# Kernel tuning notes

Measured on AMD Instinct MI355X. Metric: run time of the kernel, lower is better.

Reference implementation:

```python
import jax, jax.numpy as jnp
import numpy as np

B, S, H, E = 32, 4096, 512, 512

def setup_inputs() -> dict:
    key = jax.random.key(0)
    ks = jax.random.split(key, 11)
    sc = 1.0 / np.sqrt(H)
    return {
        "context": jax.random.normal(ks[0], (B, S, H), jnp.float32),
        "h": jax.random.normal(ks[1], (B, H), jnp.float32),
        "x": jax.random.normal(ks[2], (B, E), jnp.float32),
        "We": jax.random.normal(ks[3], (H, H), jnp.float32) * sc,
        "be": jax.random.normal(ks[4], (H,), jnp.float32) * sc,
        "Wd": jax.random.normal(ks[5], (H, H), jnp.float32) * sc,
        "bd": jax.random.normal(ks[6], (H,), jnp.float32) * sc,
        "Wv": jax.random.normal(ks[7], (H,), jnp.float32) * sc,
        "bv": jax.random.normal(ks[8], (1,), jnp.float32) * sc,
        "Wr": jax.random.normal(ks[9], (2 * H, 2 * H + E), jnp.float32) * (1.0 / np.sqrt(2 * H + E)),
        "br": jax.random.normal(ks[10], (2 * H,), jnp.float32) * sc,
    }

def reference(context, h, x, We, be, Wd, bd, Wv, bv, Wr, br):
    # gamma_encoder: [B,S,H]; gamma_decoder: [B,1,H]
    ge = jnp.einsum('bsh,kh->bsk', context, We) + be
    gd = h @ Wd.T + bd
    # additive scores -> [B,S]
    scores = jnp.einsum('bsh,h->bs', jnp.tanh(ge + gd[:, None, :]), Wv) + bv[0]
    weights = jax.nn.softmax(scores, axis=1)
    # context vector c_t: [B,H]
    c_t = jnp.einsum('bs,bsh->bh', weights, context)
    # linear_r on [c_t, h, x] -> [B,2H]
    r_t = jnp.concatenate([c_t, h, x], axis=1) @ Wr.T + br
    # maxout over pairs: view [B,H,2].max(-1)
    output = jnp.max(r_t.reshape(-1, r_t.shape[1] // 2, 2), axis=2)
    return (output, weights)
```

## Files before the change

### kernel.cpp

```cpp
#include <hip/hip_runtime.h>

typedef __attribute__((ext_vector_type(8))) short bf16x8;
typedef __attribute__((ext_vector_type(16))) float f32x16;

typedef __attribute__((address_space(3))) unsigned int lds_u32;
typedef __attribute__((address_space(1))) unsigned int glb_u32;

__device__ inline unsigned int cvt_pk_bf16(float lo, float hi){
  unsigned int r;
  asm("v_cvt_pk_bf16_f32 %0, %1, %2" : "=v"(r) : "v"(lo), "v"(hi));
  return r;
}
__device__ inline bf16x8 pack8(float4 a, float4 b){
  union { unsigned int u[4]; bf16x8 v; } r;
  r.u[0]=cvt_pk_bf16(a.x,a.y); r.u[1]=cvt_pk_bf16(a.z,a.w);
  r.u[2]=cvt_pk_bf16(b.x,b.y); r.u[3]=cvt_pk_bf16(b.z,b.w);
  return r.v;
}
__device__ inline float fast_tanh(float x){
  float e = __builtin_amdgcn_exp2f(x * 2.8853900817779268f);
  return 1.0f - 2.0f * __builtin_amdgcn_rcpf(e + 1.0f);
}
#define LOG2E 1.4426950408889634f

__global__ __launch_bounds__(256) void we_conv(const float* __restrict__ We,
                                               uint4* __restrict__ weFrag){
  int gid = blockIdx.x * 256 + threadIdx.x;
  int l  = gid & 63;
  int hc = gid >> 10;
  int colv = (hc >> 1)*32 + (l & 31);
  int k = ((hc & 1) << 8) + ((gid >> 6) & 15)*16 + (l >> 5)*8;
  const float4* src = (const float4*)(We + colv*512 + k);
  float4 f0 = src[0], f1 = src[1];
  weFrag[gid] = make_uint4(cvt_pk_bf16(f0.x,f0.y), cvt_pk_bf16(f0.z,f0.w),
                           cvt_pk_bf16(f1.x,f1.y), cvt_pk_bf16(f1.z,f1.w));
}

__global__ __launch_bounds__(256) void gd_kernel(const float* __restrict__ hvec,
                                                 const float* __restrict__ Wd,
                                                 const float* __restrict__ bd,
                                                 const float* __restrict__ be,
                                                 float* __restrict__ gd){
  __shared__ float hs[512];
  int b = blockIdx.x >> 2, kc = blockIdx.x & 3;
  int tid = threadIdx.x;
  hs[tid]       = hvec[b*512 + tid];
  hs[tid + 256] = hvec[b*512 + 256 + tid];
  __syncthreads();
  int k  = kc*128 + (tid >> 1);
  int hh = (tid & 1) * 256;
  const float4* wrow = (const float4*)(Wd + (size_t)k*512 + hh);
  const float4* hv4  = (const float4*)(hs + hh);
  float acc = 0.f;
  #pragma unroll 8
  for (int i = 0; i < 64; ++i){
    float4 w = wrow[i]; float4 u = hv4[i];
    acc += w.x*u.x + w.y*u.y + w.z*u.z + w.w*u.w;
  }
  acc += __shfl_xor(acc, 1);
  if ((tid & 1) == 0) gd[b*512 + k] = acc + bd[k] + be[k];
}

__global__ __launch_bounds__(256, 2) void score_kernel(
    const float* __restrict__ ctx, const char* __restrict__ weFrag,
    const float* __restrict__ gd, const float* __restrict__ Wv,
    float* __restrict__ scores, unsigned int* __restrict__ ctp,
    float* __restrict__ MS){
  __shared__ char lds[40960];
  float* gdwv = (float*)(lds + 24576);
  float* scl  = (float*)(lds + 32768);
  float* wl   = (float*)(lds + 33280);
  float* redp = (float*)(lds + 33792);

  const int tid  = threadIdx.x;
  const int wid  = tid >> 6;
  const int lane = tid & 63;
  const int bid  = blockIdx.x;
  const int row0 = bid * 128;
  const int b    = bid >> 5;
  const int col  = lane & 31;
  const int hi   = lane >> 5;

  if (tid < 128) ((float4*)gdwv)[tid] = ((const float4*)(gd + b*512))[tid];
  else           ((float4*)gdwv)[tid] = ((const float4*)Wv)[tid - 128];

  bf16x8 afrag[32];
  {
    const float4* ap = (const float4*)(ctx + (size_t)(row0 + wid*32 + col)*512 + hi*8);
    #pragma unroll
    for (int t = 0; t < 32; ++t)
      afrag[t] = pack8(ap[t*4], ap[t*4 + 1]);
  }

  asm volatile("s_waitcnt lgkmcnt(0)" ::: "memory");

  #define ISSUE_Q(QC) do { \
    const char* _g = weFrag + ((size_t)((QC) >> 1))*16384 + ((QC) & 1)*8192 \
                     + wid*2048 + lane*16; \
    char* _l = lds + ((QC) % 3)*8192 + wid*2048; \
    __builtin_amdgcn_global_load_lds((const glb_u32*)_g, (lds_u32*)_l, 16, 0, 0); \
    __builtin_amdgcn_global_load_lds((const glb_u32*)(_g + 1024), \
                                     (lds_u32*)(_l + 1024), 16, 0, 0); \
  } while(0)

  ISSUE_Q(0);
  ISSUE_Q(1);

  f32x16 acc;
  float sc[16];
  #pragma unroll
  for (int r = 0; r < 16; ++r) sc[r] = 0.f;

  for (int nc = 0; nc < 16; ++nc){
    #pragma unroll
    for (int r = 0; r < 16; ++r) acc[r] = 0.f;

    #pragma unroll
    for (int j = 0; j < 4; ++j){
      const int qc = nc*4 + j;
      if (qc < 63) asm volatile("s_waitcnt vmcnt(2)" ::: "memory");
      else         asm volatile("s_waitcnt vmcnt(0)" ::: "memory");
      __builtin_amdgcn_s_barrier();
      if (qc < 62) ISSUE_Q(qc + 2);
      {
        const char* bb = lds + (qc % 3)*8192 + lane*16;
        __builtin_amdgcn_s_setprio(1);
        #pragma unroll
        for (int t = 0; t < 8; ++t){
          bf16x8 bf = *(const bf16x8*)(bb + t*1024);
          acc = __builtin_amdgcn_mfma_f32_32x32x16_bf16(afrag[j*8 + t], bf, acc, 0, 0, 0);
        }
        __builtin_amdgcn_s_setprio(0);
      }
    }

    float gdv = gdwv[nc*32 + col];
    float wvv = gdwv[512 + nc*32 + col];
    #pragma unroll
    for (int r = 0; r < 16; ++r)
      sc[r] += fast_tanh(acc[r] + gdv) * wvv;
  }
  #undef ISSUE_Q

  #pragma unroll
  for (int r = 0; r < 16; ++r){
    #pragma unroll
    for (int m = 1; m <= 16; m <<= 1) sc[r] += __shfl_xor(sc[r], m);
  }

  __syncthreads();
  if (col == 0){
    int rbase = wid*32 + 4*hi;
    float* so = scores + row0 + rbase;
    #pragma unroll
    for (int r = 0; r < 16; ++r){
      int rr = (r & 3) + 8*(r >> 2);
      so[rr] = sc[r];
      scl[rbase + rr] = sc[r];
    }
  }
  __syncthreads();

  float M = -1e30f;
  {
    const float4* s4 = (const float4*)scl;
    #pragma unroll
    for (int i = 0; i < 32; ++i){
      float4 v = s4[i];
      M = fmaxf(M, fmaxf(fmaxf(v.x, v.y), fmaxf(v.z, v.w)));
    }
  }
  if (tid < 128){
    float w = __builtin_amdgcn_exp2f((scl[tid] - M) * LOG2E);
    wl[tid] = w;
    #pragma unroll
    for (int o = 1; o < 64; o <<= 1) w += __shfl_xor(w, o);
    if ((tid & 63) == 0) redp[tid >> 6] = w;
  }
  __syncthreads();
  float S_blk = redp[0] + redp[1];

  float cA = 0.f, cB = 0.f;
  #pragma unroll
  for (int p = 0; p < 4; ++p){
    if (wid == p){
      int rl = col;
      char* dst = lds + rl*1024;
      int swz = (rl & 7) << 4;
      #pragma unroll
      for (int t = 0; t < 32; ++t){
        union { bf16x8 v; uint4 q; } u; u.v = afrag[t];
        *(uint4*)(dst + ((t*32 + hi*16) ^ swz)) = u.q;
      }
    }
    __syncthreads();
    const float* wp = wl + p*32;
    #pragma unroll 8
    for (int r = 0; r < 32; ++r){
      unsigned int u = *(const unsigned int*)(lds + r*1024 + ((tid*4) ^ ((r & 7) << 4)));
      float cw = wp[r];
      union { unsigned int q; float f; } flo, fhi;
      flo.q = u << 16;
      fhi.q = u & 0xffff0000u;
      cA += cw * flo.f;
      cB += cw * fhi.f;
    }
    __syncthreads();
  }
  ctp[(size_t)bid*256 + tid] = cvt_pk_bf16(cA, cB);
  if (tid == 0){ MS[2*bid] = M; MS[2*bid + 1] = S_blk; }
}

__global__ __launch_bounds__(256) void combine_kernel(const unsigned int* __restrict__ ctp,
                                                      const float* __restrict__ MS,
                                                      float* __restrict__ ct,
                                                      float* __restrict__ mbuf){
  __shared__ float wsh[32];
  __shared__ float msh[2];
  int b = blockIdx.x, tid = threadIdx.x;
  if (tid < 32){
    float Mi = MS[(b*32 + tid)*2];
    float Si = MS[(b*32 + tid)*2 + 1];
    float M = Mi;
    #pragma unroll
    for (int o = 1; o < 32; o <<= 1) M = fmaxf(M, __shfl_xor(M, o));
    float w = __builtin_amdgcn_exp2f((Mi - M) * LOG2E);
    float d = w * Si;
    #pragma unroll
    for (int o = 1; o < 32; o <<= 1) d += __shfl_xor(d, o);
    wsh[tid] = w;
    if (tid == 0){ msh[0] = M; msh[1] = 1.0f / d; }
  }
  __syncthreads();
  float invd = msh[1];
  float a0 = 0.f, a1 = 0.f;
  #pragma unroll 8
  for (int i = 0; i < 32; ++i){
    unsigned int u = ctp[(size_t)(b*32 + i)*256 + tid];
    float w = wsh[i];
    union { unsigned int q; float f; } flo, fhi;
    flo.q = u << 16;
    fhi.q = u & 0xffff0000u;
    a0 += w * flo.f;
    a1 += w * fhi.f;
  }
  ((float2*)(ct + b*512))[tid] = make_float2(a0 * invd, a1 * invd);
  if (tid == 0){ mbuf[2*b] = msh[0]; mbuf[2*b + 1] = invd; }
}

__global__ __launch_bounds__(256) void weights_kernel(const float* __restrict__ scores,
                                                      const float* __restrict__ mbuf,
                                                      float* __restrict__ weights){
  int b = blockIdx.x, tid = threadIdx.x;
  float M = mbuf[2*b], invd = mbuf[2*b + 1];
  const float4* src = (const float4*)(scores + b*4096);
  float4* dst = (float4*)(weights + b*4096);
  #pragma unroll
  for (int i = 0; i < 4; ++i){
    float4 v = src[tid + i*256];
    v.x = __builtin_amdgcn_exp2f((v.x - M) * LOG2E) * invd;
    v.y = __builtin_amdgcn_exp2f((v.y - M) * LOG2E) * invd;
    v.z = __builtin_amdgcn_exp2f((v.z - M) * LOG2E) * invd;
    v.w = __builtin_amdgcn_exp2f((v.w - M) * LOG2E) * invd;
    dst[tid + i*256] = v;
  }
}

__global__ __launch_bounds__(256) void final_kernel(
    const float* __restrict__ ct, const float* __restrict__ hvec,
    const float* __restrict__ x, const float* __restrict__ Wr,
    const float* __restrict__ br, float* __restrict__ out){
  __shared__ float xs[8][1536];
  int bt = blockIdx.x >> 4;
  int it = blockIdx.x & 15;
  int tid = threadIdx.x;
  int b0 = bt * 8;
  for (int idx = tid; idx < 8*1536; idx += 256){
    int bl = idx / 1536, j = idx % 1536;
    int b = b0 + bl;
    float v = (j < 512) ? ct[b*512 + j]
            : (j < 1024) ? hvec[b*512 + (j - 512)]
            : x[b*512 + (j - 1024)];
    xs[bl][j] = v;
  }
  __syncthreads();
  int i = it*64 + (tid & 63);
  int bl0 = (tid >> 6) * 2;
  const float4* wrow = (const float4*)(Wr + (size_t)i*1536);
  const float4* x0 = (const float4*)xs[bl0];
  const float4* x1 = (const float4*)xs[bl0 + 1];
  float a0 = 0.f, a1 = 0.f;
  #pragma unroll 4
  for (int k = 0; k < 384; ++k){
    float4 w = wrow[k];
    float4 u0 = x0[k], u1 = x1[k];
    a0 += w.x*u0.x + w.y*u0.y + w.z*u0.z + w.w*u0.w;
    a1 += w.x*u1.x + w.y*u1.y + w.z*u1.z + w.w*u1.w;
  }
  float bias = br[i];
  a0 += bias; a1 += bias;
  float n0 = __shfl_xor(a0, 1);
  float n1 = __shfl_xor(a1, 1);
  if ((tid & 1) == 0){
    out[(b0 + bl0    )*512 + (i >> 1)] = fmaxf(a0, n0);
    out[(b0 + bl0 + 1)*512 + (i >> 1)] = fmaxf(a1, n1);
  }
}

extern "C" void kernel_launch(void* const* d_in, const int* in_sizes, int n_in,
                              void* d_out, int out_size, void* d_ws, size_t ws_size,
                              hipStream_t stream){
  const float* ctx  = (const float*)d_in[0];
  const float* hvec = (const float*)d_in[1];
  const float* x    = (const float*)d_in[2];
  const float* We   = (const float*)d_in[3];
  const float* be   = (const float*)d_in[4];
  const float* Wd   = (const float*)d_in[5];
  const float* bd   = (const float*)d_in[6];
  const float* Wv   = (const float*)d_in[7];
  const float* Wr   = (const float*)d_in[9];
  const float* br   = (const float*)d_in[10];

  float* out     = (float*)d_out;
  float* weights = out + 32*512;

  char* ws = (char*)d_ws;
  char* weFrag   = ws;
  float* scores  = (float*)(ws + (512 << 10));
  unsigned int* ctp = (unsigned int*)(ws + (1024 << 10));
  float* MS      = (float*)(ws + (2 << 20));
  float* mbuf    = (float*)(ws + (2 << 20) + (16 << 10));
  float* ct      = (float*)(ws + (2 << 20) + (32 << 10));
  float* gd      = (float*)(ws + (2 << 20) + (96 << 10));

  we_conv<<<128, 256, 0, stream>>>(We, (uint4*)weFrag);
  gd_kernel<<<128, 256, 0, stream>>>(hvec, Wd, bd, be, gd);
  score_kernel<<<1024, 256, 0, stream>>>(ctx, weFrag, gd, Wv, scores, ctp, MS);
  combine_kernel<<<32, 256, 0, stream>>>(ctp, MS, ct, mbuf);
  weights_kernel<<<32, 256, 0, stream>>>(scores, mbuf, weights);
  final_kernel<<<64, 256, 0, stream>>>(ct, hvec, x, Wr, br, out);
}
```

Measured before the change: 194.1 us.

## Split score GEMM K dimension across two wave groups with 512-thread blocks

The score kernel now uses 512 threads per block. Each row group of 32 rows is handled by two waves that each cover half of the K dimension, so each wave holds 16 A fragments instead of 32, which cuts register pressure and allows more resident waves. Partial accumulators are combined through a new LDS exchange buffer before the tanh step, and the We fragment layout is reordered to match. The context partials are now stored as fp32 per column rather than packed bf16, which doubles that workspace and adds an extra barrier per N chunk.

```diff
diff --git a/kernel.cpp b/kernel.cpp
--- a/kernel.cpp
+++ b/kernel.cpp
@@ -26,10 +26,14 @@
 __global__ __launch_bounds__(256) void we_conv(const float* __restrict__ We,
                                                uint4* __restrict__ weFrag){
   int gid = blockIdx.x * 256 + threadIdx.x;
-  int l  = gid & 63;
-  int hc = gid >> 10;
-  int colv = (hc >> 1)*32 + (l & 31);
-  int k = ((hc & 1) << 8) + ((gid >> 6) & 15)*16 + (l >> 5)*8;
+  int l   = gid & 63;
+  int rec = gid >> 6;
+  int nc  = rec >> 5;
+  int q   = (rec >> 3) & 3;
+  int s   = rec & 7;
+  int t   = (s < 4) ? (q*4 + s) : (16 + q*4 + (s - 4));
+  int colv = nc*32 + (l & 31);
+  int k = t*16 + (l >> 5)*8;
   const float4* src = (const float4*)(We + colv*512 + k);
   float4 f0 = src[0], f1 = src[1];
   weFrag[gid] = make_uint4(cvt_pk_bf16(f0.x,f0.y), cvt_pk_bf16(f0.z,f0.w),
@@ -61,46 +65,47 @@
   if ((tid & 1) == 0) gd[b*512 + k] = acc + bd[k] + be[k];
 }
 
-__global__ __launch_bounds__(256, 2) void score_kernel(
+__global__ __launch_bounds__(512, 4) void score_kernel(
     const float* __restrict__ ctx, const char* __restrict__ weFrag,
     const float* __restrict__ gd, const float* __restrict__ Wv,
-    float* __restrict__ scores, unsigned int* __restrict__ ctp,
+    float* __restrict__ scores, float* __restrict__ ctp,
     float* __restrict__ MS){
-  __shared__ char lds[40960];
+  __shared__ char lds[46592];
   float* gdwv = (float*)(lds + 24576);
-  float* scl  = (float*)(lds + 32768);
-  float* wl   = (float*)(lds + 33280);
-  float* redp = (float*)(lds + 33792);
+  char*  xbuf = lds + 28672;
+  float* scl  = (float*)(lds + 45056);
+  float* wl   = (float*)(lds + 45568);
+  float* redp = (float*)(lds + 46080);
 
   const int tid  = threadIdx.x;
   const int wid  = tid >> 6;
   const int lane = tid & 63;
+  const int rg   = wid & 3;
+  const int kh   = wid >> 2;
   const int bid  = blockIdx.x;
   const int row0 = bid * 128;
   const int b    = bid >> 5;
   const int col  = lane & 31;
   const int hi   = lane >> 5;
 
-  if (tid < 128) ((float4*)gdwv)[tid] = ((const float4*)(gd + b*512))[tid];
-  else           ((float4*)gdwv)[tid] = ((const float4*)Wv)[tid - 128];
-
-  bf16x8 afrag[32];
+  if (tid < 128)      ((float4*)gdwv)[tid] = ((const float4*)(gd + b*512))[tid];
+  else if (tid < 256) ((float4*)gdwv)[tid] = ((const float4*)Wv)[tid - 128];
+
+  bf16x8 afrag[16];
   {
-    const float4* ap = (const float4*)(ctx + (size_t)(row0 + wid*32 + col)*512 + hi*8);
-    #pragma unroll
-    for (int t = 0; t < 32; ++t)
+    const float4* ap = (const float4*)(ctx + (size_t)(row0 + rg*32 + col)*512
+                                       + kh*256 + hi*8);
+    #pragma unroll
+    for (int t = 0; t < 16; ++t)
       afrag[t] = pack8(ap[t*4], ap[t*4 + 1]);
   }
 
   asm volatile("s_waitcnt lgkmcnt(0)" ::: "memory");
 
   #define ISSUE_Q(QC) do { \
-    const char* _g = weFrag + ((size_t)((QC) >> 1))*16384 + ((QC) & 1)*8192 \
-                     + wid*2048 + lane*16; \
-    char* _l = lds + ((QC) % 3)*8192 + wid*2048; \
+    const char* _g = weFrag + ((size_t)(QC))*8192 + wid*1024 + lane*16; \
+    char* _l = lds + ((QC) % 3)*8192 + wid*1024; \
     __builtin_amdgcn_global_load_lds((const glb_u32*)_g, (lds_u32*)_l, 16, 0, 0); \
-    __builtin_amdgcn_global_load_lds((const glb_u32*)(_g + 1024), \
-                                     (lds_u32*)(_l + 1024), 16, 0, 0); \
   } while(0)
 
   ISSUE_Q(0);
@@ -118,39 +123,54 @@
     #pragma unroll
     for (int j = 0; j < 4; ++j){
       const int qc = nc*4 + j;
-      if (qc < 63) asm volatile("s_waitcnt vmcnt(2)" ::: "memory");
+      if (qc < 63) asm volatile("s_waitcnt vmcnt(1)" ::: "memory");
       else         asm volatile("s_waitcnt vmcnt(0)" ::: "memory");
       __builtin_amdgcn_s_barrier();
       if (qc < 62) ISSUE_Q(qc + 2);
       {
-        const char* bb = lds + (qc % 3)*8192 + lane*16;
+        const char* bb = lds + (qc % 3)*8192 + kh*4096 + lane*16;
         __builtin_amdgcn_s_setprio(1);
         #pragma unroll
-        for (int t = 0; t < 8; ++t){
-          bf16x8 bf = *(const bf16x8*)(bb + t*1024);
-          acc = __builtin_amdgcn_mfma_f32_32x32x16_bf16(afrag[j*8 + t], bf, acc, 0, 0, 0);
+        for (int i = 0; i < 4; ++i){
+          bf16x8 bf = *(const bf16x8*)(bb + i*1024);
+          acc = __builtin_amdgcn_mfma_f32_32x32x16_bf16(afrag[j*4 + i], bf, acc, 0, 0, 0);
         }
         __builtin_amdgcn_s_setprio(0);
       }
     }
 
-    float gdv = gdwv[nc*32 + col];
-    float wvv = gdwv[512 + nc*32 + col];
-    #pragma unroll
-    for (int r = 0; r < 16; ++r)
-      sc[r] += fast_tanh(acc[r] + gdv) * wvv;
+    char* xb = xbuf + rg*4096;
+    if (kh){
+      #pragma unroll
+      for (int r = 0; r < 16; r += 2)
+        *(float2*)(xb + (r >> 1)*512 + lane*8) = make_float2(acc[r], acc[r+1]);
+    }
+    asm volatile("s_waitcnt lgkmcnt(0)" ::: "memory");
+    __builtin_amdgcn_s_barrier();
+    if (!kh){
+      float gdv = gdwv[nc*32 + col];
+      float wvv = gdwv[512 + nc*32 + col];
+      #pragma unroll
+      for (int r = 0; r < 16; r += 2){
+        float2 o = *(const float2*)(xb + (r >> 1)*512 + lane*8);
+        sc[r]     += fast_tanh(acc[r]     + o.x + gdv) * wvv;
+        sc[r + 1] += fast_tanh(acc[r + 1] + o.y + gdv) * wvv;
+      }
+    }
   }
   #undef ISSUE_Q
 
-  #pragma unroll
-  for (int r = 0; r < 16; ++r){
-    #pragma unroll
-    for (int m = 1; m <= 16; m <<= 1) sc[r] += __shfl_xor(sc[r], m);
-  }
-
-  __syncthreads();
-  if (col == 0){
-    int rbase = wid*32 + 4*hi;
+  if (!kh){
+    #pragma unroll
+    for (int r = 0; r < 16; ++r){
+      #pragma unroll
+      for (int m = 1; m <= 16; m <<= 1) sc[r] += __shfl_xor(sc[r], m);
+    }
+  }
+
+  __syncthreads();
+  if (!kh && col == 0){
+    int rbase = rg*32 + 4*hi;
     float* so = scores + row0 + rbase;
     #pragma unroll
     for (int r = 0; r < 16; ++r){
@@ -161,57 +181,52 @@
   }
   __syncthreads();
 
-  float M = -1e30f;
-  {
+  if (tid < 128){
+    float M = -1e30f;
     const float4* s4 = (const float4*)scl;
     #pragma unroll
     for (int i = 0; i < 32; ++i){
       float4 v = s4[i];
       M = fmaxf(M, fmaxf(fmaxf(v.x, v.y), fmaxf(v.z, v.w)));
     }
-  }
-  if (tid < 128){
     float w = __builtin_amdgcn_exp2f((scl[tid] - M) * LOG2E);
     wl[tid] = w;
-    #pragma unroll
-    for (int o = 1; o < 64; o <<= 1) w += __shfl_xor(w, o);
-    if ((tid & 63) == 0) redp[tid >> 6] = w;
-  }
-  __syncthreads();
-  float S_blk = redp[0] + redp[1];
-
-  float cA = 0.f, cB = 0.f;
+    float d = w;
+    #pragma unroll
+    for (int o = 1; o < 64; o <<= 1) d += __shfl_xor(d, o);
+    if ((tid & 63) == 0) redp[tid >> 6] = d;
+    if (tid == 0) MS[2*bid] = M;
+  }
+  __syncthreads();
+  if (tid == 0) MS[2*bid + 1] = redp[0] + redp[1];
+
+  float ctp1 = 0.f;
   #pragma unroll
   for (int p = 0; p < 4; ++p){
-    if (wid == p){
+    if (rg == p){
       int rl = col;
       char* dst = lds + rl*1024;
       int swz = (rl & 7) << 4;
       #pragma unroll
-      for (int t = 0; t < 32; ++t){
+      for (int t = 0; t < 16; ++t){
         union { bf16x8 v; uint4 q; } u; u.v = afrag[t];
-        *(uint4*)(dst + ((t*32 + hi*16) ^ swz)) = u.q;
+        *(uint4*)(dst + ((((kh*16 + t)*32) + hi*16) ^ swz)) = u.q;
       }
     }
     __syncthreads();
     const float* wp = wl + p*32;
     #pragma unroll 8
     for (int r = 0; r < 32; ++r){
-      unsigned int u = *(const unsigned int*)(lds + r*1024 + ((tid*4) ^ ((r & 7) << 4)));
-      float cw = wp[r];
-      union { unsigned int q; float f; } flo, fhi;
-      flo.q = u << 16;
-      fhi.q = u & 0xffff0000u;
-      cA += cw * flo.f;
-      cB += cw * fhi.f;
+      unsigned int u = *(const unsigned short*)(lds + r*1024 + ((tid*2) ^ ((r & 7) << 4)));
+      union { unsigned int q; float f; } fv; fv.q = u << 16;
+      ctp1 += wp[r] * fv.f;
     }
     __syncthreads();
   }
-  ctp[(size_t)bid*256 + tid] = cvt_pk_bf16(cA, cB);
-  if (tid == 0){ MS[2*bid] = M; MS[2*bid + 1] = S_blk; }
-}
-
-__global__ __launch_bounds__(256) void combine_kernel(const unsigned int* __restrict__ ctp,
+  ctp[(size_t)bid*512 + tid] = ctp1;
+}
+
+__global__ __launch_bounds__(256) void combine_kernel(const float* __restrict__ ctp,
                                                       const float* __restrict__ MS,
                                                       float* __restrict__ ct,
                                                       float* __restrict__ mbuf){
@@ -236,13 +251,9 @@
   float a0 = 0.f, a1 = 0.f;
   #pragma unroll 8
   for (int i = 0; i < 32; ++i){
-    unsigned int u = ctp[(size_t)(b*32 + i)*256 + tid];
+    float2 v = ((const float2*)(ctp + (size_t)(b*32 + i)*512))[tid];
     float w = wsh[i];
-    union { unsigned int q; float f; } flo, fhi;
-    flo.q = u << 16;
-    fhi.q = u & 0xffff0000u;
-    a0 += w * flo.f;
-    a1 += w * fhi.f;
+    a0 += w * v.x; a1 += w * v.y;
   }
   ((float2*)(ct + b*512))[tid] = make_float2(a0 * invd, a1 * invd);
   if (tid == 0){ mbuf[2*b] = msh[0]; mbuf[2*b + 1] = invd; }
@@ -327,15 +338,15 @@
   char* ws = (char*)d_ws;
   char* weFrag   = ws;
   float* scores  = (float*)(ws + (512 << 10));
-  unsigned int* ctp = (unsigned int*)(ws + (1024 << 10));
-  float* MS      = (float*)(ws + (2 << 20));
-  float* mbuf    = (float*)(ws + (2 << 20) + (16 << 10));
-  float* ct      = (float*)(ws + (2 << 20) + (32 << 10));
-  float* gd      = (float*)(ws + (2 << 20) + (96 << 10));
+  float* ctp     = (float*)(ws + (1024 << 10));
+  float* MS      = (float*)(ws + (3 << 20));
+  float* mbuf    = (float*)(ws + (3 << 20) + (16 << 10));
+  float* ct      = (float*)(ws + (3 << 20) + (32 << 10));
+  float* gd      = (float*)(ws + (3 << 20) + (96 << 10));
 
   we_conv<<<128, 256, 0, stream>>>(We, (uint4*)weFrag);
   gd_kernel<<<128, 256, 0, stream>>>(hvec, Wd, bd, be, gd);
-  score_kernel<<<1024, 256, 0, stream>>>(ctx, weFrag, gd, Wv, scores, ctp, MS);
+  score_kernel<<<1024, 512, 0, stream>>>(ctx, weFrag, gd, Wv, scores, ctp, MS);
   combine_kernel<<<32, 256, 0, stream>>>(ctp, MS, ct, mbuf);
   weights_kernel<<<32, 256, 0, stream>>>(scores, mbuf, weights);
   final_kernel<<<64, 256, 0, stream>>>(ct, hvec, x, Wr, br, out);
```

Result: slower. 208.8 us (+7.6%).
